# Performance work log

Hardware: AMD Instinct MI355X
Metric: run time of the kernel (lower is better)

## Reference

```python
import jax, jax.numpy as jnp
import numpy as np

N, E, IN_FEATS, D, H, DIST_DIM, NBOUND = 10000, 160000, 128, 64, 4, 32, 31

def setup_inputs() -> dict:
    key = jax.random.key(0)
    ks = jax.random.split(key, 16)
    gain = 5.0 / 3.0  # tanh gain
    def xavier(k, shape):
        # xavier_normal over the last two dims (fan_in, fan_out) as torch does per-slice
        fan_in, fan_out = shape[-2], shape[-1]
        std = gain * np.sqrt(2.0 / (fan_in + fan_out))
        return jax.random.normal(k, shape, dtype=jnp.float32) * std
    inp = {
        'feat': jax.random.normal(ks[0], (N, IN_FEATS), dtype=jnp.float32),
        'locations': jax.random.normal(ks[1], (N, 3), dtype=jnp.float32),
        'src': jax.random.randint(ks[2], (E,), 0, N),
        'dst': jax.random.randint(ks[3], (E,), 0, N),
        'inter_ids': jax.random.randint(ks[4], (E, H), 0, N),
        'W_fc': xavier(ks[5], (IN_FEATS, H * D)),
        'embed_table': jax.random.normal(ks[6], (NBOUND + 1, DIST_DIM), dtype=jnp.float32),
        'G': xavier(ks[7], (H, DIST_DIM, D)),
        'attn_fc1': xavier(ks[8], (H, 2 * D, D)),
        'attn_fc2': xavier(ks[9], (H, 2 * D, D)),
        'attn_fc3': xavier(ks[10], (H, 2 * D, D)),
        'attn_fc': xavier(ks[11], (H, 3 * D, D)),
        'attn_out': xavier(ks[12], (H, D, 1)),
        'boundaries': jnp.linspace(0.1, 3.1, NBOUND).astype(jnp.float32),
    }
    return inp


def reference(feat, locations, W_fc, embed_table, G, attn_fc1, attn_fc2, attn_fc3,
              attn_fc, attn_out, boundaries, src, dst, inter_ids):
    n = feat.shape[0]
    h = (feat @ W_fc).reshape(n, H, D)                      # [N,H,D]
    pos = locations                                          # [N,3]
    src_pos = pos[src]                                       # [E,3]
    dst_pos = pos[dst]                                       # [E,3]
    inter_pos = pos[inter_ids]                               # [E,H,3]
    h_src = h[src]                                           # [E,H,D]
    h_dst = h[dst]                                           # [E,H,D]
    head_idx = jnp.arange(H)[None, :]
    inter_h = h[inter_ids, head_idx, :]                      # [E,H,D] per-head gather

    e_count = src.shape[0]
    dist1 = jnp.broadcast_to(jnp.linalg.norm(dst_pos - src_pos, axis=-1)[:, None], (e_count, H))
    dist2 = jnp.linalg.norm(dst_pos[:, None, :] - inter_pos, axis=-1)   # [E,H]
    dist_ = jnp.linalg.norm(src_pos[:, None, :] - inter_pos, axis=-1)   # [E,H]

    def dist_embed(dist):
        idx = jnp.searchsorted(boundaries, dist, side='left')  # torch.bucketize(right=False)
        e = embed_table[idx]                                   # [E,H,DIST_DIM]
        return jnp.einsum('ehk,hkd->ehd', e, G)                # [E,H,D]

    de1 = dist_embed(dist1)
    de2 = dist_embed(dist2)
    de_ = dist_embed(dist_)

    d1 = jnp.einsum('ehk,hkd->ehd', jnp.concatenate([h_src, de1], axis=-1), attn_fc1)
    d2 = jnp.einsum('ehk,hkd->ehd', jnp.concatenate([inter_h, de2], axis=-1), attn_fc2)
    d3 = jnp.einsum('ehk,hkd->ehd', jnp.concatenate([h_dst, de_], axis=-1), attn_fc3)

    h_c = jnp.tanh(jnp.einsum('ehk,hkd->ehd', jnp.concatenate([d1, d2, d3], axis=-1), attn_fc))
    e_score = jnp.einsum('ehd,hdo->eho', h_c, attn_out)[..., 0]        # [E,H]

    # edge softmax grouped by destination node
    m = jax.ops.segment_max(e_score, dst, num_segments=n)              # [N,H]
    ex = jnp.exp(e_score - m[dst])
    den = jax.ops.segment_sum(ex, dst, num_segments=n)                 # [N,H]
    a = ex / den[dst]                                                  # [E,H]

    ft = jax.ops.segment_sum(a[:, :, None] * h_src, dst, num_segments=n)  # [N,H,D]
    rst = jnp.mean(ft, axis=1)                                          # merge='mean' -> [N,D]
    return rst
```

## Files before the change

kernel.cpp:

```cpp
#include <hip/hip_runtime.h>
#include <hip/hip_fp16.h>
#include <math.h>

#define N_NODES 10000
#define E_EDGES 160000
#define DMODEL 64
#define H 4
#define NBOUND 31
#define QREC 1024

typedef _Float16 half8 __attribute__((ext_vector_type(8)));
typedef float floatx4 __attribute__((ext_vector_type(4)));

__global__ __launch_bounds__(256) void prep_pre1_cvt_kernel(
    const float* __restrict__ fc1, const float* __restrict__ fc2,
    const float* __restrict__ fc3, const float* __restrict__ fcc,
    float* __restrict__ Bws, const float* __restrict__ pos,
    float4* __restrict__ pos4, int* __restrict__ counts,
    const float* __restrict__ feat, __half* __restrict__ feat16) {
  __shared__ __align__(16) float S[12288];
  int bi = blockIdx.x;
  int tid = threadIdx.x;
  if (bi >= 52) {
    int t = (bi - 52) * 256 + tid;
    float4 v = *(const float4*)(feat + t * 4);
    union { uint2 u; __half2 h[2]; } st;
    st.h[0] = __floats2half2_rn(v.x, v.y);
    st.h[1] = __floats2half2_rn(v.z, v.w);
    *(uint2*)&feat16[t * 4] = st.u;
    return;
  }
  if (bi >= 12) {
    int n = (bi - 12) * 256 + tid;
    if (n < N_NODES) {
      counts[n] = 0;
      pos4[n] = make_float4(pos[n * 3], pos[n * 3 + 1], pos[n * 3 + 2], 0.f);
    }
    return;
  }
  int kh = bi;
  int k = kh >> 2, h = kh & 3;
  const float* fck = (k == 0) ? fc1 : (k == 1) ? fc2 : fc3;
  fck += h * 128 * 64;
  const float* F = fcc + h * 192 * 64 + k * 64 * 64;
  #pragma unroll
  for (int u = 0; u < 8; ++u)
    ((float4*)S)[u * 256 + tid] = ((const float4*)fck)[u * 256 + tid];
  #pragma unroll
  for (int u = 0; u < 4; ++u)
    ((float4*)(S + 8192))[u * 256 + tid] = ((const float4*)F)[u * 256 + tid];
  __syncthreads();
  int j = tid & 63, ig = tid >> 6;
  #pragma unroll
  for (int rg = 0; rg < 8; ++rg) {
    int i0 = ig * 32 + rg * 4;
    float a0 = 0.f, a1 = 0.f, a2 = 0.f, a3 = 0.f;
    #pragma unroll
    for (int t4 = 0; t4 < 16; ++t4) {
      float4 f0 = *(const float4*)&S[(i0 + 0) * 64 + t4 * 4];
      float4 f1 = *(const float4*)&S[(i0 + 1) * 64 + t4 * 4];
      float4 f2 = *(const float4*)&S[(i0 + 2) * 64 + t4 * 4];
      float4 f3 = *(const float4*)&S[(i0 + 3) * 64 + t4 * 4];
      float b0 = S[8192 + (t4 * 4 + 0) * 64 + j];
      float b1 = S[8192 + (t4 * 4 + 1) * 64 + j];
      float b2 = S[8192 + (t4 * 4 + 2) * 64 + j];
      float b3 = S[8192 + (t4 * 4 + 3) * 64 + j];
      a0 += f0.x * b0 + f0.y * b1 + f0.z * b2 + f0.w * b3;
      a1 += f1.x * b0 + f1.y * b1 + f1.z * b2 + f1.w * b3;
      a2 += f2.x * b0 + f2.y * b1 + f2.z * b2 + f2.w * b3;
      a3 += f3.x * b0 + f3.y * b1 + f3.z * b2 + f3.w * b3;
    }
    Bws[kh * 8192 + (i0 + 0) * 64 + j] = a0;
    Bws[kh * 8192 + (i0 + 1) * 64 + j] = a1;
    Bws[kh * 8192 + (i0 + 2) * 64 + j] = a2;
    Bws[kh * 8192 + (i0 + 3) * 64 + j] = a3;
  }
}

__device__ __forceinline__ int didx(const float* __restrict__ bnd2, float d) {
  int g = (int)(d * 10.0f);
  g = (g < 0) ? 0 : ((g > 31) ? 31 : g);
  g += (bnd2[g + 1] < d) ? 1 : 0;
  g -= (bnd2[g] >= d) ? 1 : 0;
  return g;
}

__global__ __launch_bounds__(256) void pre2_dist_kernel(
    const float* __restrict__ Wfc, const float* __restrict__ G,
    const float* __restrict__ emb, const float* __restrict__ Bws,
    __half* __restrict__ bigWT, __half* __restrict__ U16,
    const int* __restrict__ src, const int* __restrict__ dst,
    const int* __restrict__ inter, const float4* __restrict__ pos4,
    const float* __restrict__ boundaries, int* __restrict__ counts,
    int* __restrict__ widx) {
  __shared__ __align__(16) float S[9216];
  int bi = blockIdx.x;
  int tid = threadIdx.x;
  if (bi >= 60) {
    if (tid < NBOUND) S[tid + 1] = boundaries[tid];
    if (tid == NBOUND) { S[0] = -INFINITY; S[32] = INFINITY; }
    __syncthreads();
    int g = (bi - 60) * 256 + tid;
    int e = g >> 2, h = g & 3;
    int s = src[e], t = dst[e];
    int it = inter[g];
    float4 ps = pos4[s], pt = pos4[t], pi = pos4[it];
    float dx = pt.x - ps.x, dy = pt.y - ps.y, dz = pt.z - ps.z;
    float dist1 = sqrtf(dx * dx + dy * dy + dz * dz);
    float ax = pt.x - pi.x, ay = pt.y - pi.y, az = pt.z - pi.z;
    float dist2 = sqrtf(ax * ax + ay * ay + az * az);
    float bx = ps.x - pi.x, by = ps.y - pi.y, bz = ps.z - pi.z;
    float dist_ = sqrtf(bx * bx + by * by + bz * bz);
    int idx1 = didx(S, dist1);
    int idx2 = didx(S, dist2);
    int idx_ = didx(S, dist_);
    widx[g] = idx1 | (idx2 << 5) | (idx_ << 10);
    if (h == 0) atomicAdd(&counts[t], 1);
    return;
  }
  int kh = bi / 5, role = bi % 5;
  int k = kh >> 2, h = kh & 3;
  int j = tid & 63;
  if (role < 4) {
    int r0 = role * 32;
    #pragma unroll
    for (int u = 0; u < 4; ++u)
      ((float4*)S)[u * 256 + tid] = ((const float4*)(Bws + kh * 8192))[u * 256 + tid];
    #pragma unroll
    for (int u = 0; u < 2; ++u) {
      int fi = u * 256 + tid;
      int i = fi >> 4, c4 = fi & 15;
      ((float4*)(S + 4096))[fi] =
          ((const float4*)(Wfc + (r0 + i) * 256 + h * 64))[c4];
    }
    __syncthreads();
    int ig = tid >> 6;
    int i0 = ig * 8;
    #pragma unroll
    for (int g4 = 0; g4 < 2; ++g4) {
      int ib = i0 + g4 * 4;
      float a0 = 0.f, a1 = 0.f, a2 = 0.f, a3 = 0.f;
      #pragma unroll
      for (int t4 = 0; t4 < 16; ++t4) {
        float4 f0 = *(const float4*)&S[4096 + (ib + 0) * 64 + t4 * 4];
        float4 f1 = *(const float4*)&S[4096 + (ib + 1) * 64 + t4 * 4];
        float4 f2 = *(const float4*)&S[4096 + (ib + 2) * 64 + t4 * 4];
        float4 f3 = *(const float4*)&S[4096 + (ib + 3) * 64 + t4 * 4];
        float b0 = S[(t4 * 4 + 0) * 64 + j];
        float b1 = S[(t4 * 4 + 1) * 64 + j];
        float b2 = S[(t4 * 4 + 2) * 64 + j];
        float b3 = S[(t4 * 4 + 3) * 64 + j];
        a0 += f0.x * b0 + f0.y * b1 + f0.z * b2 + f0.w * b3;
        a1 += f1.x * b0 + f1.y * b1 + f1.z * b2 + f1.w * b3;
        a2 += f2.x * b0 + f2.y * b1 + f2.z * b2 + f2.w * b3;
        a3 += f3.x * b0 + f3.y * b1 + f3.z * b2 + f3.w * b3;
      }
      __half hv[4] = {__float2half(a0), __float2half(a1), __float2half(a2),
                      __float2half(a3)};
      *(uint2*)&bigWT[((k + 1) * 256 + h * 64 + j) * 128 + r0 + ib] =
          *(uint2*)hv;
    }
    if (k == 0) {
      #pragma unroll
      for (int u = 0; u < 8; ++u) {
        int idx = u * 256 + tid;
        int i = idx >> 6, jj = idx & 63;
        bigWT[(h * 64 + jj) * 128 + r0 + i] = __float2half(S[4096 + idx]);
      }
    }
  } else {
    #pragma unroll
    for (int u = 0; u < 4; ++u)
      ((float4*)S)[u * 256 + tid] =
          ((const float4*)(Bws + kh * 8192 + 4096))[u * 256 + tid];
    #pragma unroll
    for (int u = 0; u < 2; ++u)
      ((float4*)(S + 4096))[u * 256 + tid] =
          ((const float4*)(G + h * 2048))[u * 256 + tid];
    ((float4*)(S + 6144))[tid] = ((const float4*)emb)[tid];
    __syncthreads();
    int wv = tid >> 6;
    #pragma unroll
    for (int rg = 0; rg < 2; ++rg) {
      int g0 = wv * 8 + rg * 4;
      float a0 = 0.f, a1 = 0.f, a2 = 0.f, a3 = 0.f;
      #pragma unroll
      for (int t4 = 0; t4 < 16; ++t4) {
        float4 f0 = *(const float4*)&S[4096 + (g0 + 0) * 64 + t4 * 4];
        float4 f1 = *(const float4*)&S[4096 + (g0 + 1) * 64 + t4 * 4];
        float4 f2 = *(const float4*)&S[4096 + (g0 + 2) * 64 + t4 * 4];
        float4 f3 = *(const float4*)&S[4096 + (g0 + 3) * 64 + t4 * 4];
        float b0 = S[(t4 * 4 + 0) * 64 + j];
        float b1 = S[(t4 * 4 + 1) * 64 + j];
        float b2 = S[(t4 * 4 + 2) * 64 + j];
        float b3 = S[(t4 * 4 + 3) * 64 + j];
        a0 += f0.x * b0 + f0.y * b1 + f0.z * b2 + f0.w * b3;
        a1 += f1.x * b0 + f1.y * b1 + f1.z * b2 + f1.w * b3;
        a2 += f2.x * b0 + f2.y * b1 + f2.z * b2 + f2.w * b3;
        a3 += f3.x * b0 + f3.y * b1 + f3.z * b2 + f3.w * b3;
      }
      S[7168 + (g0 + 0) * 64 + j] = a0;
      S[7168 + (g0 + 1) * 64 + j] = a1;
      S[7168 + (g0 + 2) * 64 + j] = a2;
      S[7168 + (g0 + 3) * 64 + j] = a3;
    }
    __syncthreads();
    #pragma unroll
    for (int rg = 0; rg < 2; ++rg) {
      int e0 = wv * 8 + rg * 4;
      float a0 = 0.f, a1 = 0.f, a2 = 0.f, a3 = 0.f;
      #pragma unroll
      for (int t4 = 0; t4 < 8; ++t4) {
        float4 f0 = *(const float4*)&S[6144 + (e0 + 0) * 32 + t4 * 4];
        float4 f1 = *(const float4*)&S[6144 + (e0 + 1) * 32 + t4 * 4];
        float4 f2 = *(const float4*)&S[6144 + (e0 + 2) * 32 + t4 * 4];
        float4 f3 = *(const float4*)&S[6144 + (e0 + 3) * 32 + t4 * 4];
        float b0 = S[7168 + (t4 * 4 + 0) * 64 + j];
        float b1 = S[7168 + (t4 * 4 + 1) * 64 + j];
        float b2 = S[7168 + (t4 * 4 + 2) * 64 + j];
        float b3 = S[7168 + (t4 * 4 + 3) * 64 + j];
        a0 += f0.x * b0 + f0.y * b1 + f0.z * b2 + f0.w * b3;
        a1 += f1.x * b0 + f1.y * b1 + f1.z * b2 + f1.w * b3;
        a2 += f2.x * b0 + f2.y * b1 + f2.z * b2 + f2.w * b3;
        a3 += f3.x * b0 + f3.y * b1 + f3.z * b2 + f3.w * b3;
      }
      int base = k * 8192 + h * 2048;
      U16[base + (e0 + 0) * 64 + j] = __float2half(a0);
      U16[base + (e0 + 1) * 64 + j] = __float2half(a1);
      U16[base + (e0 + 2) * 64 + j] = __float2half(a2);
      U16[base + (e0 + 3) * 64 + j] = __float2half(a3);
    }
  }
}

__global__ __launch_bounds__(256) void scan_gemm_kernel(
    const int* __restrict__ counts, int* __restrict__ starts,
    int* __restrict__ cursor, const __half* __restrict__ feat16,
    const __half* __restrict__ bigWT, __half* __restrict__ qall) {
  int bi = blockIdx.x;
  int tid = threadIdx.x;
  if (bi == 0) {
    __shared__ int lds[256];
    int base = tid * 40;
    int loc[40];
    int s = 0;
    #pragma unroll
    for (int u = 0; u < 40; ++u) {
      int i = base + u;
      int v = (i < N_NODES) ? counts[i] : 0;
      loc[u] = s;
      s += v;
    }
    lds[tid] = s;
    __syncthreads();
    int inc = s;
    for (int off = 1; off < 256; off <<= 1) {
      int y = (tid >= off) ? lds[tid - off] : 0;
      __syncthreads();
      inc += y;
      lds[tid] = inc;
      __syncthreads();
    }
    int excl = inc - s;
    #pragma unroll
    for (int u = 0; u < 40; ++u) {
      int i = base + u;
      if (i < N_NODES) {
        int v = excl + loc[u];
        starts[i] = v;
        cursor[i] = v;
      }
    }
    if (tid == 255) starts[N_NODES] = inc;
    return;
  }
  int gb = bi - 1;
  int bx = gb % 157, by = gb / 157;
  int wv = tid >> 6, l = tid & 63;
  int m0 = bx * 64 + wv * 16;
  int n0 = by * 256;
  int lm = l & 15, lk = (l >> 4) * 8;
  int arow = m0 + lm;
  if (arow >= N_NODES) arow = N_NODES - 1;
  const _Float16* fp = (const _Float16*)feat16 + arow * 128 + lk;
  const _Float16* bp = (const _Float16*)bigWT + lk;
  half8 a[4];
  #pragma unroll
  for (int kt = 0; kt < 4; ++kt) a[kt] = *(const half8*)(fp + kt * 32);
  int mrow = m0 + (l >> 4) * 4;
  #pragma unroll
  for (int nt = 0; nt < 16; ++nt) {
    floatx4 acc = (floatx4){0.f, 0.f, 0.f, 0.f};
    #pragma unroll
    for (int kt = 0; kt < 4; ++kt) {
      half8 b = *(const half8*)(bp + (n0 + nt * 16 + lm) * 128 + kt * 32);
      acc = __builtin_amdgcn_mfma_f32_16x16x32_f16(a[kt], b, acc, 0, 0, 0);
    }
    int dd = nt * 16 + lm;
    int off = (by == 0) ? ((dd & 63) * 4 + (dd >> 6)) : (by * 256 + dd);
    #pragma unroll
    for (int r4 = 0; r4 < 4; ++r4) {
      int m = mrow + r4;
      if (m < N_NODES) qall[m * QREC + off] = __float2half(acc[r4]);
    }
  }
}

__device__ __forceinline__ float dpp_row_sum16(float v) {
  int x;
  x = __builtin_amdgcn_update_dpp(0, __float_as_int(v), 0x128, 0xf, 0xf, true);
  v += __int_as_float(x);
  x = __builtin_amdgcn_update_dpp(0, __float_as_int(v), 0x124, 0xf, 0xf, true);
  v += __int_as_float(x);
  x = __builtin_amdgcn_update_dpp(0, __float_as_int(v), 0x122, 0xf, 0xf, true);
  v += __int_as_float(x);
  x = __builtin_amdgcn_update_dpp(0, __float_as_int(v), 0x121, 0xf, 0xf, true);
  v += __int_as_float(x);
  return v;
}

union H4u { uint2 u; __half2 h[2]; };

__global__ __launch_bounds__(256) void score_fill_kernel(
    const int* __restrict__ src, const int* __restrict__ dst,
    const int* __restrict__ inter, const int* __restrict__ widx,
    const __half* __restrict__ qall, const __half* __restrict__ U16,
    const float* __restrict__ aout, int* __restrict__ cursor,
    float* __restrict__ exsc, int* __restrict__ esrc) {
  int tid = threadIdx.x;
  int wv = tid >> 6, lane = tid & 63;
  int h = lane >> 4, c = lane & 15;
  int e = blockIdx.x * 4 + wv;
  int s = src[e], t = dst[e];
  int it = inter[e * 4 + h];
  int wp = widx[e * 4 + h];
  int idx1 = wp & 31, idx2 = (wp >> 5) & 31, idx_ = (wp >> 10) & 31;
  H4u A, B, C, X, Y, Z;
  A.u = *(const uint2*)(qall + s * QREC + 256 + h * 64 + c * 4);
  B.u = *(const uint2*)(qall + it * QREC + 512 + h * 64 + c * 4);
  C.u = *(const uint2*)(qall + t * QREC + 768 + h * 64 + c * 4);
  X.u = *(const uint2*)(U16 + (h * 32 + idx1) * 64 + c * 4);
  Y.u = *(const uint2*)(U16 + 8192 + (h * 32 + idx2) * 64 + c * 4);
  Z.u = *(const uint2*)(U16 + 16384 + (h * 32 + idx_) * 64 + c * 4);
  const float4 a4 = *((const float4*)(aout + h * 64) + c);
  __half2 z0 = __hadd2(__hadd2(A.h[0], B.h[0]), __hadd2(C.h[0], X.h[0]));
  z0 = __hadd2(z0, __hadd2(Y.h[0], Z.h[0]));
  __half2 z1 = __hadd2(__hadd2(A.h[1], B.h[1]), __hadd2(C.h[1], X.h[1]));
  z1 = __hadd2(z1, __hadd2(Y.h[1], Z.h[1]));
  float2 f0 = __half22float2(z0);
  float2 f1 = __half22float2(z1);
  const float K = 2.885390082f;
  float p0 = __builtin_amdgcn_exp2f(f0.x * K);
  float p1 = __builtin_amdgcn_exp2f(f0.y * K);
  float p2 = __builtin_amdgcn_exp2f(f1.x * K);
  float p3 = __builtin_amdgcn_exp2f(f1.y * K);
  float r0 = __builtin_amdgcn_rcpf(p0 + 1.0f);
  float r1 = __builtin_amdgcn_rcpf(p1 + 1.0f);
  float r2 = __builtin_amdgcn_rcpf(p2 + 1.0f);
  float r3 = __builtin_amdgcn_rcpf(p3 + 1.0f);
  float dot = a4.x * r0;
  dot = fmaf(a4.y, r1, dot);
  dot = fmaf(a4.z, r2, dot);
  dot = fmaf(a4.w, r3, dot);
  float asum = (a4.x + a4.y) + (a4.z + a4.w);
  float v = fmaf(-2.0f, dot, asum);
  v = dpp_row_sum16(v);
  int p = 0;
  if (lane == 0) p = atomicAdd(&cursor[t], 1);
  p = __shfl(p, 0);
  if (c == 0) exsc[p * 4 + h] = __expf(v);
  if (lane == 0) esrc[p] = s;
}

__device__ __forceinline__ float4 h4_to_f4(uint2 u) {
  union { uint2 ui; __half2 h[2]; } cc;
  cc.ui = u;
  float2 a = __half22float2(cc.h[0]);
  float2 b = __half22float2(cc.h[1]);
  return make_float4(a.x, a.y, b.x, b.y);
}

__global__ __launch_bounds__(256) void agg_kernel(
    const int* __restrict__ starts, const int* __restrict__ esrc,
    const float* __restrict__ exsc, const __half* __restrict__ qall,
    float* __restrict__ out) {
  __shared__ float4 sm_num[4][64];
  __shared__ float4 sm_den[4];
  int tid = threadIdx.x;
  int w = tid >> 6, lane = tid & 63;
  int n = blockIdx.x;
  int b = starts[n], e_end = starts[n + 1];
  float4 num = make_float4(0.f, 0.f, 0.f, 0.f);
  float4 den = make_float4(0.f, 0.f, 0.f, 0.f);
  int i = b + w;
  float4 exA = make_float4(0.f, 0.f, 0.f, 0.f);
  float4 exB = make_float4(0.f, 0.f, 0.f, 0.f);
  uint2 hA = {0, 0}, hB = {0, 0};
  if (i < e_end) {
    exA = *(const float4*)(exsc + i * 4);
    hA = *(const uint2*)(qall + esrc[i] * QREC + lane * 4);
  }
  if (i + 4 < e_end) {
    exB = *(const float4*)(exsc + (i + 4) * 4);
    hB = *(const uint2*)(qall + esrc[i + 4] * QREC + lane * 4);
  }
  while (i < e_end) {
    int i2 = i + 8, i3 = i + 12;
    float4 exC = make_float4(0.f, 0.f, 0.f, 0.f);
    float4 exD = make_float4(0.f, 0.f, 0.f, 0.f);
    uint2 hC = {0, 0}, hD = {0, 0};
    if (i2 < e_end) {
      exC = *(const float4*)(exsc + i2 * 4);
      hC = *(const uint2*)(qall + esrc[i2] * QREC + lane * 4);
    }
    if (i3 < e_end) {
      exD = *(const float4*)(exsc + i3 * 4);
      hD = *(const uint2*)(qall + esrc[i3] * QREC + lane * 4);
    }
    float4 hvA = h4_to_f4(hA);
    num.x += exA.x * hvA.x;
    num.y += exA.y * hvA.y;
    num.z += exA.z * hvA.z;
    num.w += exA.w * hvA.w;
    den.x += exA.x; den.y += exA.y; den.z += exA.z; den.w += exA.w;
    float4 hvB = h4_to_f4(hB);
    num.x += exB.x * hvB.x;
    num.y += exB.y * hvB.y;
    num.z += exB.z * hvB.z;
    num.w += exB.w * hvB.w;
    den.x += exB.x; den.y += exB.y; den.z += exB.z; den.w += exB.w;
    i = i2;
    exA = exC; hA = hC;
    exB = exD; hB = hD;
  }
  sm_num[w][lane] = num;
  if (lane == 0) sm_den[w] = den;
  __syncthreads();
  if (tid < 64) {
    float4 n0 = sm_num[0][tid], n1 = sm_num[1][tid];
    float4 n2 = sm_num[2][tid], n3 = sm_num[3][tid];
    float4 d0 = sm_den[0], d1 = sm_den[1], d2 = sm_den[2], d3 = sm_den[3];
    float4 ns = make_float4(n0.x + n1.x + n2.x + n3.x, n0.y + n1.y + n2.y + n3.y,
                            n0.z + n1.z + n2.z + n3.z, n0.w + n1.w + n2.w + n3.w);
    float4 ds = make_float4(d0.x + d1.x + d2.x + d3.x, d0.y + d1.y + d2.y + d3.y,
                            d0.z + d1.z + d2.z + d3.z, d0.w + d1.w + d2.w + d3.w);
    float r = 0.f;
    if (e_end > b)
      r = 0.25f * (ns.x / ds.x + ns.y / ds.y + ns.z / ds.z + ns.w / ds.w);
    out[n * 64 + tid] = r;
  }
}

extern "C" void kernel_launch(void* const* d_in, const int* in_sizes, int n_in,
                              void* d_out, int out_size, void* d_ws,
                              size_t ws_size, hipStream_t stream) {
  const float* feat = (const float*)d_in[0];
  const float* loc = (const float*)d_in[1];
  const int* src = (const int*)d_in[2];
  const int* dst = (const int*)d_in[3];
  const int* inter = (const int*)d_in[4];
  const float* Wfc = (const float*)d_in[5];
  const float* emb = (const float*)d_in[6];
  const float* G = (const float*)d_in[7];
  const float* fc1 = (const float*)d_in[8];
  const float* fc2 = (const float*)d_in[9];
  const float* fc3 = (const float*)d_in[10];
  const float* fcc = (const float*)d_in[11];
  const float* aout = (const float*)d_in[12];
  const float* bnd = (const float*)d_in[13];
  float* out = (float*)d_out;

  __half* qall = (__half*)d_ws;
  __half* bigWT = qall + N_NODES * QREC;
  __half* U16 = bigWT + 1024 * 128;
  __half* feat16 = U16 + 3 * H * 2048;
  float* Bws = (float*)(feat16 + N_NODES * 128);
  float4* pos4 = (float4*)(Bws + 12 * 8192);
  float* exsc = (float*)(pos4 + N_NODES);
  int* widx = (int*)(exsc + E_EDGES * 4);
  int* counts = widx + E_EDGES * 4;
  int* starts = counts + N_NODES;
  int* cursor = starts + N_NODES + 1;
  int* esrc = cursor + N_NODES;

  prep_pre1_cvt_kernel<<<1302, 256, 0, stream>>>(fc1, fc2, fc3, fcc, Bws, loc,
                                                 pos4, counts, feat, feat16);
  pre2_dist_kernel<<<60 + E_EDGES * 4 / 256, 256, 0, stream>>>(
      Wfc, G, emb, Bws, bigWT, U16, src, dst, inter, pos4, bnd, counts, widx);
  scan_gemm_kernel<<<1 + 157 * 4, 256, 0, stream>>>(counts, starts, cursor,
                                                    feat16, bigWT, qall);
  score_fill_kernel<<<E_EDGES / 4, 256, 0, stream>>>(
      src, dst, inter, widx, qall, U16, aout, cursor, exsc, esrc);
  agg_kernel<<<N_NODES, 256, 0, stream>>>(starts, esrc, exsc, qall, out);
}
```

Before: 214.6 us.

## Stage GEMM output in LDS, batch two items per thread/wave across kernels

The distance kernel now handles two edge-head items per thread with half the blocks. The GEMM epilogue stages the fp16 results in shared memory and writes full rows with 16-byte stores instead of scattered 2-byte stores. score_fill handles two edges per wave to raise memory-level parallelism, and the agg loop is restructured to issue four gathers per iteration instead of using a software-pipelined prefetch. These changes trade fewer blocks and a little more register and LDS use for fewer, wider memory transactions.

```diff
diff --git a/kernel.cpp b/kernel.cpp
--- a/kernel.cpp
+++ b/kernel.cpp
@@ -85,6 +85,28 @@
   return g;
 }
 
+__device__ __forceinline__ void dist_one(
+    const float* __restrict__ S, const int* __restrict__ src,
+    const int* __restrict__ dst, const int* __restrict__ inter,
+    const float4* __restrict__ pos4, int* __restrict__ counts,
+    int* __restrict__ widx, int g) {
+  int e = g >> 2, h = g & 3;
+  int s = src[e], t = dst[e];
+  int it = inter[g];
+  float4 ps = pos4[s], pt = pos4[t], pi = pos4[it];
+  float dx = pt.x - ps.x, dy = pt.y - ps.y, dz = pt.z - ps.z;
+  float dist1 = sqrtf(dx * dx + dy * dy + dz * dz);
+  float ax = pt.x - pi.x, ay = pt.y - pi.y, az = pt.z - pi.z;
+  float dist2 = sqrtf(ax * ax + ay * ay + az * az);
+  float bx = ps.x - pi.x, by = ps.y - pi.y, bz = ps.z - pi.z;
+  float dist_ = sqrtf(bx * bx + by * by + bz * bz);
+  int idx1 = didx(S, dist1);
+  int idx2 = didx(S, dist2);
+  int idx_ = didx(S, dist_);
+  widx[g] = idx1 | (idx2 << 5) | (idx_ << 10);
+  if (h == 0) atomicAdd(&counts[t], 1);
+}
+
 __global__ __launch_bounds__(256) void pre2_dist_kernel(
     const float* __restrict__ Wfc, const float* __restrict__ G,
     const float* __restrict__ emb, const float* __restrict__ Bws,
@@ -100,22 +122,9 @@
     if (tid < NBOUND) S[tid + 1] = boundaries[tid];
     if (tid == NBOUND) { S[0] = -INFINITY; S[32] = INFINITY; }
     __syncthreads();
-    int g = (bi - 60) * 256 + tid;
-    int e = g >> 2, h = g & 3;
-    int s = src[e], t = dst[e];
-    int it = inter[g];
-    float4 ps = pos4[s], pt = pos4[t], pi = pos4[it];
-    float dx = pt.x - ps.x, dy = pt.y - ps.y, dz = pt.z - ps.z;
-    float dist1 = sqrtf(dx * dx + dy * dy + dz * dz);
-    float ax = pt.x - pi.x, ay = pt.y - pi.y, az = pt.z - pi.z;
-    float dist2 = sqrtf(ax * ax + ay * ay + az * az);
-    float bx = ps.x - pi.x, by = ps.y - pi.y, bz = ps.z - pi.z;
-    float dist_ = sqrtf(bx * bx + by * by + bz * bz);
-    int idx1 = didx(S, dist1);
-    int idx2 = didx(S, dist2);
-    int idx_ = didx(S, dist_);
-    widx[g] = idx1 | (idx2 << 5) | (idx_ << 10);
-    if (h == 0) atomicAdd(&counts[t], 1);
+    int g0 = (bi - 60) * 512 + tid;
+    dist_one(S, src, dst, inter, pos4, counts, widx, g0);
+    dist_one(S, src, dst, inter, pos4, counts, widx, g0 + 256);
     return;
   }
   int kh = bi / 5, role = bi % 5;
@@ -233,6 +242,8 @@
   }
 }
 
+#define EROW 264
+
 __global__ __launch_bounds__(256) void scan_gemm_kernel(
     const int* __restrict__ counts, int* __restrict__ starts,
     int* __restrict__ cursor, const __half* __restrict__ feat16,
@@ -274,6 +285,7 @@
     if (tid == 255) starts[N_NODES] = inc;
     return;
   }
+  __shared__ __align__(16) __half Esm[4][16][EROW];
   int gb = bi - 1;
   int bx = gb % 157, by = gb / 157;
   int wv = tid >> 6, l = tid & 63;
@@ -287,7 +299,6 @@
   half8 a[4];
   #pragma unroll
   for (int kt = 0; kt < 4; ++kt) a[kt] = *(const half8*)(fp + kt * 32);
-  int mrow = m0 + (l >> 4) * 4;
   #pragma unroll
   for (int nt = 0; nt < 16; ++nt) {
     floatx4 acc = (floatx4){0.f, 0.f, 0.f, 0.f};
@@ -297,11 +308,21 @@
       acc = __builtin_amdgcn_mfma_f32_16x16x32_f16(a[kt], b, acc, 0, 0, 0);
     }
     int dd = nt * 16 + lm;
-    int off = (by == 0) ? ((dd & 63) * 4 + (dd >> 6)) : (by * 256 + dd);
+    int o = (by == 0) ? ((dd & 63) * 4 + (dd >> 6)) : dd;
     #pragma unroll
     for (int r4 = 0; r4 < 4; ++r4) {
-      int m = mrow + r4;
-      if (m < N_NODES) qall[m * QREC + off] = __float2half(acc[r4]);
+      Esm[wv][(l >> 4) * 4 + r4][o] = __float2half(acc[r4]);
+    }
+  }
+  __syncthreads();
+  int row = l >> 2;
+  int j0 = (l & 3) * 64;
+  int m = m0 + row;
+  if (m < N_NODES) {
+    #pragma unroll
+    for (int u = 0; u < 8; ++u) {
+      uint4 v = *(const uint4*)&Esm[wv][row][j0 + u * 8];
+      *(uint4*)&qall[m * QREC + by * 256 + j0 + u * 8] = v;
     }
   }
 }
@@ -321,28 +342,8 @@
 
 union H4u { uint2 u; __half2 h[2]; };
 
-__global__ __launch_bounds__(256) void score_fill_kernel(
-    const int* __restrict__ src, const int* __restrict__ dst,
-    const int* __restrict__ inter, const int* __restrict__ widx,
-    const __half* __restrict__ qall, const __half* __restrict__ U16,
-    const float* __restrict__ aout, int* __restrict__ cursor,
-    float* __restrict__ exsc, int* __restrict__ esrc) {
-  int tid = threadIdx.x;
-  int wv = tid >> 6, lane = tid & 63;
-  int h = lane >> 4, c = lane & 15;
-  int e = blockIdx.x * 4 + wv;
-  int s = src[e], t = dst[e];
-  int it = inter[e * 4 + h];
-  int wp = widx[e * 4 + h];
-  int idx1 = wp & 31, idx2 = (wp >> 5) & 31, idx_ = (wp >> 10) & 31;
-  H4u A, B, C, X, Y, Z;
-  A.u = *(const uint2*)(qall + s * QREC + 256 + h * 64 + c * 4);
-  B.u = *(const uint2*)(qall + it * QREC + 512 + h * 64 + c * 4);
-  C.u = *(const uint2*)(qall + t * QREC + 768 + h * 64 + c * 4);
-  X.u = *(const uint2*)(U16 + (h * 32 + idx1) * 64 + c * 4);
-  Y.u = *(const uint2*)(U16 + 8192 + (h * 32 + idx2) * 64 + c * 4);
-  Z.u = *(const uint2*)(U16 + 16384 + (h * 32 + idx_) * 64 + c * 4);
-  const float4 a4 = *((const float4*)(aout + h * 64) + c);
+__device__ __forceinline__ float tanh_dot(H4u A, H4u B, H4u C, H4u X, H4u Y,
+                                          H4u Z, float4 a4) {
   __half2 z0 = __hadd2(__hadd2(A.h[0], B.h[0]), __hadd2(C.h[0], X.h[0]));
   z0 = __hadd2(z0, __hadd2(Y.h[0], Z.h[0]));
   __half2 z1 = __hadd2(__hadd2(A.h[1], B.h[1]), __hadd2(C.h[1], X.h[1]));
@@ -363,13 +364,59 @@
   dot = fmaf(a4.z, r2, dot);
   dot = fmaf(a4.w, r3, dot);
   float asum = (a4.x + a4.y) + (a4.z + a4.w);
-  float v = fmaf(-2.0f, dot, asum);
-  v = dpp_row_sum16(v);
-  int p = 0;
-  if (lane == 0) p = atomicAdd(&cursor[t], 1);
-  p = __shfl(p, 0);
-  if (c == 0) exsc[p * 4 + h] = __expf(v);
-  if (lane == 0) esrc[p] = s;
+  return fmaf(-2.0f, dot, asum);
+}
+
+__global__ __launch_bounds__(256) void score_fill_kernel(
+    const int* __restrict__ src, const int* __restrict__ dst,
+    const int* __restrict__ inter, const int* __restrict__ widx,
+    const __half* __restrict__ qall, const __half* __restrict__ U16,
+    const float* __restrict__ aout, int* __restrict__ cursor,
+    float* __restrict__ exsc, int* __restrict__ esrc) {
+  int tid = threadIdx.x;
+  int wv = tid >> 6, lane = tid & 63;
+  int h = lane >> 4, c = lane & 15;
+  int e0 = blockIdx.x * 8 + wv * 2;
+  int e1 = e0 + 1;
+  int s0 = src[e0], t0 = dst[e0];
+  int s1 = src[e1], t1 = dst[e1];
+  int it0 = inter[e0 * 4 + h], it1 = inter[e1 * 4 + h];
+  int wp0 = widx[e0 * 4 + h], wp1 = widx[e1 * 4 + h];
+  int i10 = wp0 & 31, i20 = (wp0 >> 5) & 31, i_0 = (wp0 >> 10) & 31;
+  int i11 = wp1 & 31, i21 = (wp1 >> 5) & 31, i_1 = (wp1 >> 10) & 31;
+  H4u A0, B0, C0, X0, Y0, Z0, A1, B1, C1, X1, Y1, Z1;
+  A0.u = *(const uint2*)(qall + s0 * QREC + 256 + h * 64 + c * 4);
+  A1.u = *(const uint2*)(qall + s1 * QREC + 256 + h * 64 + c * 4);
+  B0.u = *(const uint2*)(qall + it0 * QREC + 512 + h * 64 + c * 4);
+  B1.u = *(const uint2*)(qall + it1 * QREC + 512 + h * 64 + c * 4);
+  C0.u = *(const uint2*)(qall + t0 * QREC + 768 + h * 64 + c * 4);
+  C1.u = *(const uint2*)(qall + t1 * QREC + 768 + h * 64 + c * 4);
+  X0.u = *(const uint2*)(U16 + (h * 32 + i10) * 64 + c * 4);
+  X1.u = *(const uint2*)(U16 + (h * 32 + i11) * 64 + c * 4);
+  Y0.u = *(const uint2*)(U16 + 8192 + (h * 32 + i20) * 64 + c * 4);
+  Y1.u = *(const uint2*)(U16 + 8192 + (h * 32 + i21) * 64 + c * 4);
+  Z0.u = *(const uint2*)(U16 + 16384 + (h * 32 + i_0) * 64 + c * 4);
+  Z1.u = *(const uint2*)(U16 + 16384 + (h * 32 + i_1) * 64 + c * 4);
+  const float4 a4 = *((const float4*)(aout + h * 64) + c);
+  float v0 = tanh_dot(A0, B0, C0, X0, Y0, Z0, a4);
+  float v1 = tanh_dot(A1, B1, C1, X1, Y1, Z1, a4);
+  v0 = dpp_row_sum16(v0);
+  v1 = dpp_row_sum16(v1);
+  int p0 = 0, p1 = 0;
+  if (lane == 0) {
+    p0 = atomicAdd(&cursor[t0], 1);
+    p1 = atomicAdd(&cursor[t1], 1);
+  }
+  p0 = __shfl(p0, 0);
+  p1 = __shfl(p1, 0);
+  if (c == 0) {
+    exsc[p0 * 4 + h] = __expf(v0);
+    exsc[p1 * 4 + h] = __expf(v1);
+  }
+  if (lane == 0) {
+    esrc[p0] = s0;
+    esrc[p1] = s1;
+  }
 }
 
 __device__ __forceinline__ float4 h4_to_f4(uint2 u) {
@@ -393,45 +440,29 @@
   float4 num = make_float4(0.f, 0.f, 0.f, 0.f);
   float4 den = make_float4(0.f, 0.f, 0.f, 0.f);
   int i = b + w;
-  float4 exA = make_float4(0.f, 0.f, 0.f, 0.f);
-  float4 exB = make_float4(0.f, 0.f, 0.f, 0.f);
-  uint2 hA = {0, 0}, hB = {0, 0};
-  if (i < e_end) {
-    exA = *(const float4*)(exsc + i * 4);
-    hA = *(const uint2*)(qall + esrc[i] * QREC + lane * 4);
-  }
-  if (i + 4 < e_end) {
-    exB = *(const float4*)(exsc + (i + 4) * 4);
-    hB = *(const uint2*)(qall + esrc[i + 4] * QREC + lane * 4);
-  }
   while (i < e_end) {
-    int i2 = i + 8, i3 = i + 12;
-    float4 exC = make_float4(0.f, 0.f, 0.f, 0.f);
-    float4 exD = make_float4(0.f, 0.f, 0.f, 0.f);
-    uint2 hC = {0, 0}, hD = {0, 0};
-    if (i2 < e_end) {
-      exC = *(const float4*)(exsc + i2 * 4);
-      hC = *(const uint2*)(qall + esrc[i2] * QREC + lane * 4);
-    }
-    if (i3 < e_end) {
-      exD = *(const float4*)(exsc + i3 * 4);
-      hD = *(const uint2*)(qall + esrc[i3] * QREC + lane * 4);
-    }
-    float4 hvA = h4_to_f4(hA);
-    num.x += exA.x * hvA.x;
-    num.y += exA.y * hvA.y;
-    num.z += exA.z * hvA.z;
-    num.w += exA.w * hvA.w;
-    den.x += exA.x; den.y += exA.y; den.z += exA.z; den.w += exA.w;
-    float4 hvB = h4_to_f4(hB);
-    num.x += exB.x * hvB.x;
-    num.y += exB.y * hvB.y;
-    num.z += exB.z * hvB.z;
-    num.w += exB.w * hvB.w;
-    den.x += exB.x; den.y += exB.y; den.z += exB.z; den.w += exB.w;
-    i = i2;
-    exA = exC; hA = hC;
-    exB = exD; hB = hD;
+    float4 ex[4];
+    uint2 hr[4];
+    #pragma unroll
+    for (int u = 0; u < 4; ++u) {
+      ex[u] = make_float4(0.f, 0.f, 0.f, 0.f);
+      hr[u] = make_uint2(0, 0);
+      int idx = i + u * 4;
+      if (idx < e_end) {
+        ex[u] = *(const float4*)(exsc + idx * 4);
+        hr[u] = *(const uint2*)(qall + esrc[idx] * QREC + lane * 4);
+      }
+    }
+    #pragma unroll
+    for (int u = 0; u < 4; ++u) {
+      float4 hv = h4_to_f4(hr[u]);
+      num.x += ex[u].x * hv.x;
+      num.y += ex[u].y * hv.y;
+      num.z += ex[u].z * hv.z;
+      num.w += ex[u].w * hv.w;
+      den.x += ex[u].x; den.y += ex[u].y; den.z += ex[u].z; den.w += ex[u].w;
+    }
+    i += 16;
   }
   sm_num[w][lane] = num;
   if (lane == 0) sm_den[w] = den;
@@ -485,11 +516,11 @@
 
   prep_pre1_cvt_kernel<<<1302, 256, 0, stream>>>(fc1, fc2, fc3, fcc, Bws, loc,
                                                  pos4, counts, feat, feat16);
-  pre2_dist_kernel<<<60 + E_EDGES * 4 / 256, 256, 0, stream>>>(
+  pre2_dist_kernel<<<60 + 1250, 256, 0, stream>>>(
       Wfc, G, emb, Bws, bigWT, U16, src, dst, inter, pos4, bnd, counts, widx);
   scan_gemm_kernel<<<1 + 157 * 4, 256, 0, stream>>>(counts, starts, cursor,
                                                     feat16, bigWT, qall);
-  score_fill_kernel<<<E_EDGES / 4, 256, 0, stream>>>(
+  score_fill_kernel<<<E_EDGES / 8, 256, 0, stream>>>(
       src, dst, inter, widx, qall, U16, aout, cursor, exsc, esrc);
   agg_kernel<<<N_NODES, 256, 0, stream>>>(starts, esrc, exsc, qall, out);
 }
```

New measurement: 209.7 us. -2.3%, faster.
